# Optimization experiments

Measured on AMD Instinct MI355X. Metric: run time of the kernel, lower is better.

Reference implementation:

```python
import jax, jax.numpy as jnp
import numpy as np

IN_CH, OUT_CH, K = 4096, 4096, 64
C, F = IN_CH // K, OUT_CH // K  # 64, 64
BS = 256


def setup_inputs() -> dict:
    key = jax.random.key(0)
    k1, k2 = jax.random.split(key)
    x = jax.random.normal(k1, (BS, IN_CH), dtype=jnp.float32)
    stdv = 1.0 / float(np.sqrt(C))  # matches torch init: uniform(-1/sqrt(in_channels), ...)
    weights = jax.random.uniform(k2, (F, C, K), dtype=jnp.float32, minval=-stdv, maxval=stdv)
    return {"x": x, "weights": weights}


def reference(x, weights):
    # Faithful, batched version of Linear_BC_func.forward:
    #   per sample: ifft(fft(w, 'ortho') * fft(x, 'backward'), 'ortho').real, summed over C.
    # The per-sample Python loop and the C-sum are fused: sum over C is done in the
    # frequency domain (linearity of ifft), and the batch is handled by one einsum.
    bs = x.shape[0]
    f, c, k = weights.shape
    xk = x.reshape(bs, c, k)
    Wf = jnp.fft.fft(weights, norm="ortho")      # (F, C, K) complex64
    Xf = jnp.fft.fft(xk, norm="backward")        # (BS, C, K) complex64
    Sf = jnp.einsum("fck,bck->bfk", Wf, Xf)      # sum over C in frequency domain
    out = jnp.fft.ifft(Sf, norm="ortho").real.astype(jnp.float32)  # torch .float() keeps real part
    return out.reshape(bs, f * k)
```

## Files before the change

kernel.cpp:

```cpp
#include <hip/hip_runtime.h>


#define KDIM 4096

typedef __attribute__((ext_vector_type(8)))  short s16x8;
typedef __attribute__((ext_vector_type(4)))  float f32x4;
typedef __attribute__((ext_vector_type(16))) float f32x16;
typedef unsigned short u16;

__device__ __forceinline__ u16 f2bf(float f) {
  unsigned int u = __float_as_uint(f);
  u += 0x7FFF + ((u >> 16) & 1);
  return (u16)(u >> 16);
}

__global__ __launch_bounds__(256) void pack_kernel(const float* __restrict__ x,
                                                   u16* __restrict__ Xp) {
  __shared__ __align__(16) u16 tile[32 * 264];
  const int tid = threadIdx.x;
  const int rg  = blockIdx.x >> 4;
  const int cg  = blockIdx.x & 15;

  #pragma unroll
  for (int i = 0; i < 4; ++i) {
    int g    = i * 2048 + tid * 8;
    int row  = g >> 8;
    int kloc = g & 255;
    const float4* src = (const float4*)(x + (size_t)(rg * 32 + row) * 4096 + cg * 256 + kloc);
    float4 v0 = src[0], v1 = src[1];
    union { u16 u[8]; uint4 v; } o;
    o.u[0] = f2bf(v0.x); o.u[1] = f2bf(v0.y); o.u[2] = f2bf(v0.z); o.u[3] = f2bf(v0.w);
    o.u[4] = f2bf(v1.x); o.u[5] = f2bf(v1.y); o.u[6] = f2bf(v1.z); o.u[7] = f2bf(v1.w);
    *(uint4*)(tile + row * 264 + kloc) = o.v;
  }
  __syncthreads();

  const int lane = tid & 63;
  const int fw   = tid >> 6;
  #pragma unroll
  for (int i = 0; i < 4; ++i) {
    int fidx = i * 4 + fw;
    int cl   = fidx >> 2;
    int kk   = fidx & 3;
    int c    = cg * 4 + cl;
    uint4 v = *(const uint4*)(tile + (lane & 31) * 264 + cl * 64 + kk * 16 + (lane >> 5) * 8);
    size_t u = ((size_t)((c * 8 + rg) * 4 + kk) << 6) + lane;
    *(uint4*)(Xp + (u << 3)) = v;
  }
}

__global__ __launch_bounds__(1024, 4) void gemm_free(const u16* __restrict__ Xp,
                                                     const float* __restrict__ w,
                                                     float* __restrict__ out) {
  extern __shared__ __align__(16) char pool[];
  u16* tab = (u16*)pool;

  const int tid   = threadIdx.x;
  const int lane  = tid & 63;
  const int wid   = tid >> 6;
  const int cslot = wid & 7;
  const int half  = wid >> 3;
  const int l31   = lane & 31;
  const int lh    = lane >> 5;
  const int f     = blockIdx.x >> 2;
  const int q     = blockIdx.x & 3;
  const int rg    = q * 2 + half;

  const float* wf = w + ((size_t)f << 12);
  #pragma unroll
  for (int j = 0; j < 4; ++j) {
    int c = wid * 4 + j;
    u16 bv = f2bf(wf[(c << 6) + lane]);
    u16* T = tab + c * 576;
    #pragma unroll
    for (int m = 0; m < 8; ++m) {
      int i = (-(lane + m)) & 63;
      T[m * 72 + i] = bv;
    }
  }

  int bofs[4];
  #pragma unroll
  for (int s = 0; s < 4; ++s) {
    int i0 = (lh * 8 - l31 - 16 * s) & 63;
    bofs[s] = (i0 & 7) * 71 + i0;
  }

  const u16* abase = Xp + ((size_t)(cslot * 8 + rg) * 2048 + lane * 8);

  f32x16 acc0 = {}, acc1 = {};
  s16x8 a0, a1, a2, a3, n0, n1, n2, n3;
  a0 = *(const s16x8*)(abase);
  a1 = *(const s16x8*)(abase + 512);
  a2 = *(const s16x8*)(abase + 1024);
  a3 = *(const s16x8*)(abase + 1536);

  __syncthreads();

  #pragma unroll
  for (int t = 0; t < 8; ++t) {
    if (t < 7) {
      const u16* nb = abase + (size_t)(t + 1) * 131072;
      n0 = *(const s16x8*)(nb);
      n1 = *(const s16x8*)(nb + 512);
      n2 = *(const s16x8*)(nb + 1024);
      n3 = *(const s16x8*)(nb + 1536);
    }
    const u16* T = tab + (8 * t + cslot) * 576;
    s16x8 b0 = *(const s16x8*)(T + bofs[0]);
    s16x8 b1 = *(const s16x8*)(T + bofs[1]);
    s16x8 b2 = *(const s16x8*)(T + bofs[2]);
    s16x8 b3 = *(const s16x8*)(T + bofs[3]);
    acc0 = __builtin_amdgcn_mfma_f32_32x32x16_bf16(a0, b0, acc0, 0, 0, 0);
    acc1 = __builtin_amdgcn_mfma_f32_32x32x16_bf16(a0, b2, acc1, 0, 0, 0);
    acc0 = __builtin_amdgcn_mfma_f32_32x32x16_bf16(a1, b3, acc0, 0, 0, 0);
    acc1 = __builtin_amdgcn_mfma_f32_32x32x16_bf16(a1, b1, acc1, 0, 0, 0);
    acc0 = __builtin_amdgcn_mfma_f32_32x32x16_bf16(a2, b2, acc0, 0, 0, 0);
    acc1 = __builtin_amdgcn_mfma_f32_32x32x16_bf16(a2, b0, acc1, 0, 0, 0);
    acc0 = __builtin_amdgcn_mfma_f32_32x32x16_bf16(a3, b1, acc0, 0, 0, 0);
    acc1 = __builtin_amdgcn_mfma_f32_32x32x16_bf16(a3, b3, acc1, 0, 0, 0);
    if (t < 7) { a0 = n0; a1 = n1; a2 = n2; a3 = n3; }
  }

  __syncthreads();
  float* red = (float*)pool;

  #define WRITE_ACC(k)                                                        \
    { float* Bf = red + (size_t)(half * 4 + (k)) * 2048;                      \
      _Pragma("unroll")                                                       \
      for (int i = 0; i < 4; ++i) {                                           \
        f32x4 v0 = {acc0[4*i], acc0[4*i+1], acc0[4*i+2], acc0[4*i+3]};        \
        f32x4 v1 = {acc1[4*i], acc1[4*i+1], acc1[4*i+2], acc1[4*i+3]};        \
        *(f32x4*)(Bf + (size_t)i * 256 + lane * 4) = v0;                      \
        *(f32x4*)(Bf + (size_t)(i + 4) * 256 + lane * 4) = v1;                \
      } }
  #define ADD_ACC(k)                                                          \
    { const float* Bf = red + (size_t)(half * 4 + (k)) * 2048;                \
      _Pragma("unroll")                                                       \
      for (int i = 0; i < 4; ++i) {                                           \
        f32x4 v0 = *(const f32x4*)(Bf + (size_t)i * 256 + lane * 4);          \
        f32x4 v1 = *(const f32x4*)(Bf + (size_t)(i + 4) * 256 + lane * 4);    \
        _Pragma("unroll")                                                     \
        for (int e = 0; e < 4; ++e) {                                         \
          acc0[4*i+e] += v0[e];                                               \
          acc1[4*i+e] += v1[e];                                               \
        }                                                                     \
      } }

  if (cslot >= 4) WRITE_ACC(cslot - 4);
  __syncthreads();
  if (cslot < 4) ADD_ACC(cslot);
  __syncthreads();
  if (cslot == 2 || cslot == 3) WRITE_ACC(cslot - 2);
  __syncthreads();
  if (cslot < 2) ADD_ACC(cslot);
  __syncthreads();
  if (cslot == 1) WRITE_ACC(0);
  __syncthreads();
  if (cslot == 0) {
    ADD_ACC(0);
    const int colg = (f << 6) + l31;
    const int rowb = q * 64 + half * 32 + 4 * lh;
    #pragma unroll
    for (int r = 0; r < 16; ++r) {
      int row = rowb + (r & 3) + 8 * (r >> 2);
      out[(size_t)row * 4096 + colg]      = acc0[r];
      out[(size_t)row * 4096 + colg + 32] = acc1[r];
    }
  }
}

extern "C" void kernel_launch(void* const* d_in, const int* in_sizes, int n_in,
                              void* d_out, int out_size, void* d_ws, size_t ws_size,
                              hipStream_t stream) {
  const float* x = (const float*)d_in[0];
  const float* w = (const float*)d_in[1];
  float* out = (float*)d_out;

  u16* Xp = (u16*)d_ws;

  pack_kernel<<<128, 256, 0, stream>>>(x, Xp);
  gemm_free<<<256, 1024, 73728, stream>>>(Xp, w, out);
}
```

Baseline: 20.80 us.

## Flatten cross-wave reduction and deepen A-operand prefetch to two stages

Replaces the multi-step tree reduction of per-wave accumulators (several barriers with most waves idle) with a single store of all wave partials to LDS followed by a parallel 8-way sum where every thread produces four outputs. Also deepens the global prefetch of A fragments to a three-slot ring so loads are issued two iterations ahead. Shared memory per block grows to 128KB and register pressure rises from the extra buffered fragments.

```diff
diff --git a/kernel.cpp b/kernel.cpp
--- a/kernel.cpp
+++ b/kernel.cpp
@@ -49,11 +49,12 @@
   }
 }
 
-__global__ __launch_bounds__(1024, 4) void gemm_free(const u16* __restrict__ Xp,
-                                                     const float* __restrict__ w,
-                                                     float* __restrict__ out) {
+__global__ __launch_bounds__(1024, 4) void gemm_p2(const u16* __restrict__ Xp,
+                                                   const float* __restrict__ w,
+                                                   float* __restrict__ out) {
   extern __shared__ __align__(16) char pool[];
-  u16* tab = (u16*)pool;
+  u16*   tab = (u16*)pool;
+  float* red = (float*)pool;
 
   const int tid   = threadIdx.x;
   const int lane  = tid & 63;
@@ -88,85 +89,66 @@
 
   const u16* abase = Xp + ((size_t)(cslot * 8 + rg) * 2048 + lane * 8);
 
+  s16x8 A[3][4];
+  #pragma unroll
+  for (int kk = 0; kk < 4; ++kk) {
+    A[0][kk] = *(const s16x8*)(abase + kk * 512);
+    A[1][kk] = *(const s16x8*)(abase + 131072 + kk * 512);
+  }
+
   f32x16 acc0 = {}, acc1 = {};
-  s16x8 a0, a1, a2, a3, n0, n1, n2, n3;
-  a0 = *(const s16x8*)(abase);
-  a1 = *(const s16x8*)(abase + 512);
-  a2 = *(const s16x8*)(abase + 1024);
-  a3 = *(const s16x8*)(abase + 1536);
 
   __syncthreads();
 
   #pragma unroll
   for (int t = 0; t < 8; ++t) {
-    if (t < 7) {
-      const u16* nb = abase + (size_t)(t + 1) * 131072;
-      n0 = *(const s16x8*)(nb);
-      n1 = *(const s16x8*)(nb + 512);
-      n2 = *(const s16x8*)(nb + 1024);
-      n3 = *(const s16x8*)(nb + 1536);
+    if (t < 6) {
+      const u16* nb = abase + (size_t)(t + 2) * 131072;
+      #pragma unroll
+      for (int kk = 0; kk < 4; ++kk)
+        A[(t + 2) % 3][kk] = *(const s16x8*)(nb + kk * 512);
     }
     const u16* T = tab + (8 * t + cslot) * 576;
     s16x8 b0 = *(const s16x8*)(T + bofs[0]);
     s16x8 b1 = *(const s16x8*)(T + bofs[1]);
     s16x8 b2 = *(const s16x8*)(T + bofs[2]);
     s16x8 b3 = *(const s16x8*)(T + bofs[3]);
-    acc0 = __builtin_amdgcn_mfma_f32_32x32x16_bf16(a0, b0, acc0, 0, 0, 0);
-    acc1 = __builtin_amdgcn_mfma_f32_32x32x16_bf16(a0, b2, acc1, 0, 0, 0);
-    acc0 = __builtin_amdgcn_mfma_f32_32x32x16_bf16(a1, b3, acc0, 0, 0, 0);
-    acc1 = __builtin_amdgcn_mfma_f32_32x32x16_bf16(a1, b1, acc1, 0, 0, 0);
-    acc0 = __builtin_amdgcn_mfma_f32_32x32x16_bf16(a2, b2, acc0, 0, 0, 0);
-    acc1 = __builtin_amdgcn_mfma_f32_32x32x16_bf16(a2, b0, acc1, 0, 0, 0);
-    acc0 = __builtin_amdgcn_mfma_f32_32x32x16_bf16(a3, b1, acc0, 0, 0, 0);
-    acc1 = __builtin_amdgcn_mfma_f32_32x32x16_bf16(a3, b3, acc1, 0, 0, 0);
-    if (t < 7) { a0 = n0; a1 = n1; a2 = n2; a3 = n3; }
+    const int cu = t % 3;
+    acc0 = __builtin_amdgcn_mfma_f32_32x32x16_bf16(A[cu][0], b0, acc0, 0, 0, 0);
+    acc1 = __builtin_amdgcn_mfma_f32_32x32x16_bf16(A[cu][0], b2, acc1, 0, 0, 0);
+    acc0 = __builtin_amdgcn_mfma_f32_32x32x16_bf16(A[cu][1], b3, acc0, 0, 0, 0);
+    acc1 = __builtin_amdgcn_mfma_f32_32x32x16_bf16(A[cu][1], b1, acc1, 0, 0, 0);
+    acc0 = __builtin_amdgcn_mfma_f32_32x32x16_bf16(A[cu][2], b2, acc0, 0, 0, 0);
+    acc1 = __builtin_amdgcn_mfma_f32_32x32x16_bf16(A[cu][2], b0, acc1, 0, 0, 0);
+    acc0 = __builtin_amdgcn_mfma_f32_32x32x16_bf16(A[cu][3], b1, acc0, 0, 0, 0);
+    acc1 = __builtin_amdgcn_mfma_f32_32x32x16_bf16(A[cu][3], b3, acc1, 0, 0, 0);
   }
 
   __syncthreads();
-  float* red = (float*)pool;
-
-  #define WRITE_ACC(k)                                                        \
-    { float* Bf = red + (size_t)(half * 4 + (k)) * 2048;                      \
-      _Pragma("unroll")                                                       \
-      for (int i = 0; i < 4; ++i) {                                           \
-        f32x4 v0 = {acc0[4*i], acc0[4*i+1], acc0[4*i+2], acc0[4*i+3]};        \
-        f32x4 v1 = {acc1[4*i], acc1[4*i+1], acc1[4*i+2], acc1[4*i+3]};        \
-        *(f32x4*)(Bf + (size_t)i * 256 + lane * 4) = v0;                      \
-        *(f32x4*)(Bf + (size_t)(i + 4) * 256 + lane * 4) = v1;                \
-      } }
-  #define ADD_ACC(k)                                                          \
-    { const float* Bf = red + (size_t)(half * 4 + (k)) * 2048;                \
-      _Pragma("unroll")                                                       \
-      for (int i = 0; i < 4; ++i) {                                           \
-        f32x4 v0 = *(const f32x4*)(Bf + (size_t)i * 256 + lane * 4);          \
-        f32x4 v1 = *(const f32x4*)(Bf + (size_t)(i + 4) * 256 + lane * 4);    \
-        _Pragma("unroll")                                                     \
-        for (int e = 0; e < 4; ++e) {                                         \
-          acc0[4*i+e] += v0[e];                                               \
-          acc1[4*i+e] += v1[e];                                               \
-        }                                                                     \
-      } }
-
-  if (cslot >= 4) WRITE_ACC(cslot - 4);
+  {
+    float* slot = red + wid * 2048;
+    #pragma unroll
+    for (int i = 0; i < 4; ++i) {
+      f32x4 v0 = {acc0[4*i], acc0[4*i+1], acc0[4*i+2], acc0[4*i+3]};
+      f32x4 v1 = {acc1[4*i], acc1[4*i+1], acc1[4*i+2], acc1[4*i+3]};
+      *(f32x4*)(slot + ((i)     * 64 + lane) * 4) = v0;
+      *(f32x4*)(slot + ((i + 4) * 64 + lane) * 4) = v1;
+    }
+  }
   __syncthreads();
-  if (cslot < 4) ADD_ACC(cslot);
-  __syncthreads();
-  if (cslot == 2 || cslot == 3) WRITE_ACC(cslot - 2);
-  __syncthreads();
-  if (cslot < 2) ADD_ACC(cslot);
-  __syncthreads();
-  if (cslot == 1) WRITE_ACC(0);
-  __syncthreads();
-  if (cslot == 0) {
-    ADD_ACC(0);
-    const int colg = (f << 6) + l31;
-    const int rowb = q * 64 + half * 32 + 4 * lh;
+  {
+    const int rhalf = tid >> 9;
+    const int ii    = (tid >> 6) & 7;
+    const int sl    = tid & 63;
+    f32x4 s = {};
     #pragma unroll
-    for (int r = 0; r < 16; ++r) {
-      int row = rowb + (r & 3) + 8 * (r >> 2);
-      out[(size_t)row * 4096 + colg]      = acc0[r];
-      out[(size_t)row * 4096 + colg + 32] = acc1[r];
-    }
+    for (int cs = 0; cs < 8; ++cs)
+      s += *(const f32x4*)(red + (size_t)(rhalf * 8 + cs) * 2048 + (ii * 64 + sl) * 4);
+    const int col  = (f << 6) + (ii >> 2) * 32 + (sl & 31);
+    const int rowb = q * 64 + rhalf * 32 + 4 * (sl >> 5) + 8 * (ii & 3);
+    #pragma unroll
+    for (int e = 0; e < 4; ++e)
+      out[(size_t)(rowb + e) * 4096 + col] = s[e];
   }
 }
 
@@ -180,5 +162,5 @@
   u16* Xp = (u16*)d_ws;
 
   pack_kernel<<<128, 256, 0, stream>>>(x, Xp);
-  gemm_free<<<256, 1024, 73728, stream>>>(Xp, w, out);
+  gemm_p2<<<256, 1024, 131072, stream>>>(Xp, w, out);
 }
```

Result: faster. 19.79 us (-4.9%).
